# Kernel optimization log

Hardware: AMD Instinct MI355X
Metric: run time of the kernel (lower is better)

Reference implementation:

```python
import jax, jax.numpy as jnp
import numpy as np

EMBED_DIM = 1024
NUM_HEADS = 16
D_K = EMBED_DIM // NUM_HEADS
GAMMA = 1.0


def setup_inputs() -> dict:
    key = jax.random.key(0)
    ks = jax.random.split(key, 5)
    B, N, E = 2, 2048, EMBED_DIM
    scale = 1.0 / np.sqrt(E)
    x = jax.random.normal(ks[0], (B, N, E), dtype=jnp.float32)
    Wq = jax.random.normal(ks[1], (E, E), dtype=jnp.float32) * scale
    Wk = jax.random.normal(ks[2], (E, E), dtype=jnp.float32) * scale
    Wv = jax.random.normal(ks[3], (E, E), dtype=jnp.float32) * scale
    Wo = jax.random.normal(ks[4], (E, E), dtype=jnp.float32) * scale
    mask = jnp.ones((B, N), dtype=jnp.int32)
    return {"x": x, "Wq": Wq, "Wk": Wk, "Wv": Wv, "Wo": Wo, "mask": mask}


def _split_heads(t):
    B, N, E = t.shape
    return t.reshape(B, N, NUM_HEADS, D_K).transpose(0, 2, 1, 3)  # [B,H,N,dk]


def reference(x, Wq, Wk, Wv, Wo, mask):
    B, N, E = x.shape
    # Linear layers (bias=False): y = x @ W.T
    q = _split_heads(x @ Wq.T)
    k = _split_heads(x @ Wk.T)
    v = _split_heads(x @ Wv.T)
    # Squared L2 distance via ||q||^2 + ||k||^2 - 2 q.k (same math as (q-k)^2.sum,
    # without materializing the [B,H,N,N,dk] diff tensor).
    q_sq = jnp.sum(q * q, axis=-1)  # [B,H,N]
    k_sq = jnp.sum(k * k, axis=-1)  # [B,H,N]
    qk = jnp.einsum('bhqd,bhkd->bhqk', q, k)
    sq_dist = jnp.maximum(q_sq[..., :, None] + k_sq[..., None, :] - 2.0 * qk, 0.0)
    similarity = jnp.exp(-GAMMA * sq_dist)  # [B,H,N,N]
    # mask.unsqueeze(1).unsqueeze(2): broadcast over heads and query dim
    mask_exp = mask[:, None, None, :]  # [B,1,1,N]
    similarity = jnp.where(mask_exp == 0, jnp.float32(-1e9), similarity)
    attn = jax.nn.softmax(similarity, axis=-1)
    # dropout p=0.0 (eval) -> identity
    out = jnp.einsum('bhqk,bhkd->bhqd', attn, v)
    out = out.transpose(0, 2, 1, 3).reshape(B, N, E)
    return out @ Wo.T
```

## Files before the change

kernel.cpp:

```cpp
#include <hip/hip_runtime.h>
#include <hip/hip_bf16.h>


using bf16x8 = __attribute__((ext_vector_type(8))) __bf16;
using f32x4  = __attribute__((ext_vector_type(4))) float;
using f32x16 = __attribute__((ext_vector_type(16))) float;

typedef const __attribute__((address_space(1))) void* gas_t;
typedef __attribute__((address_space(3))) void* las_t;

#define C_LOG2E 1.4426950408889634f
#define TWO_C   2.8853900817779268f
#define NEG_INV_4C (-0.17328679513998632f)

#if __has_builtin(__builtin_amdgcn_exp2f)
#define EXP2(x) __builtin_amdgcn_exp2f(x)
#else
#define EXP2(x) __expf((x) * 0.6931471805599453f)
#endif

static __device__ __forceinline__ unsigned short f2bf(float x) {
  union { float f; unsigned u; } c; c.f = x;
  unsigned u = c.u;
  u += 0x7fffu + ((u >> 16) & 1u);
  return (unsigned short)(u >> 16);
}
static __device__ __forceinline__ float bf2f(unsigned short b) {
  union { unsigned u; float f; } c; c.u = ((unsigned)b) << 16;
  return c.f;
}
static __device__ __forceinline__ unsigned cvt_pk_bf16(float lo, float hi) {
  unsigned r;
  asm("v_cvt_pk_bf16_f32 %0, %1, %2" : "=v"(r) : "v"(lo), "v"(hi));
  return r;
}
static __device__ __forceinline__ void permlane32_swap(unsigned &a, unsigned &b) {
#if __has_builtin(__builtin_amdgcn_permlane32_swap)
  auto r = __builtin_amdgcn_permlane32_swap(a, b, false, false);
  a = r[0]; b = r[1];
#else
  asm("v_permlane32_swap_b32 %0, %1" : "+v"(a), "+v"(b));
#endif
}

#define SYNC_VM(N)                                                           \
  do {                                                                       \
    asm volatile("s_waitcnt vmcnt(" #N ") lgkmcnt(0)\n\ts_barrier" ::: "memory"); \
    __builtin_amdgcn_sched_barrier(0);                                       \
  } while (0)

__global__ __launch_bounds__(256)
void cvt_all(const float* __restrict__ x,  const float* __restrict__ wq,
             const float* __restrict__ wk, const float* __restrict__ wv,
             const float* __restrict__ wo,
             unsigned short* __restrict__ xbf, unsigned short* __restrict__ Wbf,
             float* __restrict__ FullVm, float* __restrict__ den_base,
             unsigned* __restrict__ kmax_bits) {
  const int idx = blockIdx.x * 256 + threadIdx.x;
  if (blockIdx.x == 0) {
    const int tid = threadIdx.x;
#pragma unroll
    for (int i = 0; i < 8; ++i) FullVm[tid + i * 256] = 0.f;
    if (tid < 32) kmax_bits[tid] = 0xFF800000u;
    if (tid < 2) den_base[tid] = 0.f;
  }
  const float* src; unsigned short* dst; int off;
  if (idx < 1048576) { src = x; dst = xbf; off = idx; }
  else {
    const int r = idx - 1048576;
    const int w = r >> 18;
    off = r & 262143;
    src = (w == 0) ? wq : (w == 1) ? wk : (w == 2) ? wv : wo;
    dst = Wbf + (size_t)w * 1048576u;
  }
  const float4 v = ((const float4*)src)[off];
  ushort4 o;
  o.x = f2bf(v.x); o.y = f2bf(v.y); o.z = f2bf(v.z); o.w = f2bf(v.w);
  ((ushort4*)dst)[off] = o;
}

template<int MODE>
__global__ __launch_bounds__(256)
void gemm_bt(const unsigned short* __restrict__ A,
             const unsigned short* __restrict__ Bt,
             void* __restrict__ out0, int Kdim,
             float* __restrict__ qsqp, float* __restrict__ ksqp) {
  constexpr int RING = (MODE == 0) ? 3 : 4;
  __shared__ unsigned short As[RING][4096];
  __shared__ unsigned short Bs[RING][4096];
  const int t  = threadIdx.x;
  const int m0 = blockIdx.x * 128;
  const int n0 = blockIdx.y * 128;
  const int srow = t >> 2;
  const int scol = (((t & 3) ^ (srow & 3) ^ ((srow >> 2) & 3))) * 8;
  const unsigned short* pA = A  + (size_t)(m0 + srow) * Kdim + scol;
  const unsigned short* pB = Bt + (size_t)(n0 + srow) * Kdim + scol;
  const size_t rowskip = (size_t)64 * Kdim;

  const int wave = t >> 6, lane = t & 63;
  const int wm = (wave >> 1) * 64, wn = (wave & 1) * 64;
  const int fr = lane & 15, fg = lane >> 4;
  const int fswz = fg ^ (fr & 3) ^ ((fr >> 2) & 3);
  const int aoff = (wm + fr) * 32 + fswz * 8;
  const int boff = (wn + fr) * 32 + fswz * 8;

  f32x4 acc[4][4];
#pragma unroll
  for (int mi = 0; mi < 4; ++mi)
#pragma unroll
    for (int ni = 0; ni < 4; ++ni)
      acc[mi][ni] = (f32x4){0.f, 0.f, 0.f, 0.f};

#define GSTAGE(bi, kk)                                                                                  \
  do {                                                                                                  \
    const int kc = (kk) * 32;                                                                           \
    __builtin_amdgcn_global_load_lds((gas_t)(const void*)(pA + kc),           (las_t)(void*)(As[bi] + t * 8),        16, 0, 0); \
    __builtin_amdgcn_global_load_lds((gas_t)(const void*)(pA + kc + rowskip), (las_t)(void*)(As[bi] + 2048 + t * 8), 16, 0, 0); \
    __builtin_amdgcn_global_load_lds((gas_t)(const void*)(pB + kc),           (las_t)(void*)(Bs[bi] + t * 8),        16, 0, 0); \
    __builtin_amdgcn_global_load_lds((gas_t)(const void*)(pB + kc + rowskip), (las_t)(void*)(Bs[bi] + 2048 + t * 8), 16, 0, 0); \
  } while (0)

  const int NK = Kdim >> 5;
  if constexpr (MODE == 0) {
    GSTAGE(0, 0);
    GSTAGE(1, 1);
    for (int ks = 0; ks < NK; ++ks) {
      const int cur = ks % 3;
      if (ks + 1 < NK) SYNC_VM(4); else SYNC_VM(0);
      if (ks + 2 < NK) GSTAGE((ks + 2) % 3, ks + 2);

      bf16x8 af[4], bfr[4];
#pragma unroll
      for (int mi = 0; mi < 4; ++mi) af[mi]  = *(const bf16x8*)(As[cur] + aoff + mi * 512);
#pragma unroll
      for (int ni = 0; ni < 4; ++ni) bfr[ni] = *(const bf16x8*)(Bs[cur] + boff + ni * 512);
#pragma unroll
      for (int mi = 0; mi < 4; ++mi)
#pragma unroll
        for (int ni = 0; ni < 4; ++ni)
          acc[mi][ni] = __builtin_amdgcn_mfma_f32_16x16x32_bf16(af[mi], bfr[ni], acc[mi][ni], 0, 0, 0);
    }
  } else {
    GSTAGE(0, 0);
    GSTAGE(1, 1);
    GSTAGE(2, 2);
    for (int ks = 0; ks < NK; ++ks) {
      const int cur = ks & 3;
      if (ks + 2 < NK) SYNC_VM(8);
      else if (ks + 1 < NK) SYNC_VM(4);
      else SYNC_VM(0);
      if (ks + 3 < NK) GSTAGE((ks + 3) & 3, ks + 3);

      bf16x8 af[4], bfr[4];
#pragma unroll
      for (int mi = 0; mi < 4; ++mi) af[mi]  = *(const bf16x8*)(As[cur] + aoff + mi * 512);
#pragma unroll
      for (int ni = 0; ni < 4; ++ni) bfr[ni] = *(const bf16x8*)(Bs[cur] + boff + ni * 512);
#pragma unroll
      for (int mi = 0; mi < 4; ++mi)
#pragma unroll
        for (int ni = 0; ni < 4; ++ni)
          acc[mi][ni] = __builtin_amdgcn_mfma_f32_16x16x32_bf16(af[mi], bfr[ni], acc[mi][ni], 0, 0, 0);
    }
  }
#undef GSTAGE

  if constexpr (MODE == 1) {
    float* dst = (float*)out0;
#pragma unroll
    for (int mi = 0; mi < 4; ++mi) {
      const int gm = m0 + wm + mi * 16 + fg * 4;
#pragma unroll
      for (int ni = 0; ni < 4; ++ni) {
        const int gn = n0 + wn + ni * 16 + fr;
#pragma unroll
        for (int r = 0; r < 4; ++r)
          dst[(size_t)(gm + r) * 1024 + gn] = acc[mi][ni][r];
      }
    }
    return;
  } else {
    const int wavecol = n0 + wn;
    const int zz = wavecol >> 10;
    unsigned short* outw = (unsigned short*)out0;
    if (zz < 2) {
      const float sc = (zz == 0) ? TWO_C : 1.0f;
      const float qscale = (zz == 0) ? NEG_INV_4C : -C_LOG2E;
      unsigned short* dst = outw + (size_t)zz * 4194304u;
      const int hh = (wavecol & 1023) >> 6;
      float* dq = (zz == 0) ? qsqp : ksqp;
#pragma unroll
      for (int mi = 0; mi < 4; ++mi) {
        const int gm = m0 + wm + mi * 16 + fg * 4;
        float s0 = 0.f, s1 = 0.f, s2 = 0.f, s3 = 0.f;
#pragma unroll
        for (int ni = 0; ni < 4; ++ni) {
          const int col = (wavecol + ni * 16 + fr) & 1023;
          const unsigned short u0 = f2bf(acc[mi][ni][0] * sc);
          const unsigned short u1 = f2bf(acc[mi][ni][1] * sc);
          const unsigned short u2 = f2bf(acc[mi][ni][2] * sc);
          const unsigned short u3 = f2bf(acc[mi][ni][3] * sc);
          dst[(size_t)(gm + 0) * 1024 + col] = u0;
          dst[(size_t)(gm + 1) * 1024 + col] = u1;
          dst[(size_t)(gm + 2) * 1024 + col] = u2;
          dst[(size_t)(gm + 3) * 1024 + col] = u3;
          const float r0 = bf2f(u0), r1 = bf2f(u1), r2 = bf2f(u2), r3 = bf2f(u3);
          s0 += r0 * r0; s1 += r1 * r1; s2 += r2 * r2; s3 += r3 * r3;
        }
#pragma unroll
        for (int off2 = 1; off2 < 16; off2 <<= 1) {
          s0 += __shfl_xor(s0, off2);
          s1 += __shfl_xor(s1, off2);
          s2 += __shfl_xor(s2, off2);
          s3 += __shfl_xor(s3, off2);
        }
        if (fr == 0) {
          const int bb = gm >> 11;
          float4 o4;
          o4.x = s0 * qscale; o4.y = s1 * qscale;
          o4.z = s2 * qscale; o4.w = s3 * qscale;
          *(float4*)(dq + (bb * 16 + hh) * 2048 + (gm & 2047)) = o4;
        }
      }
    } else {
#pragma unroll
      for (int mi = 0; mi < 4; ++mi) {
        const int gm = m0 + wm + mi * 16 + fg * 4;
#pragma unroll
        for (int ni = 0; ni < 4; ++ni) {
          const int gn = n0 + wn + ni * 16 + fr;
          const int col = gn & 1023;
          ushort4 o4;
          o4.x = f2bf(acc[mi][ni][0]); o4.y = f2bf(acc[mi][ni][1]);
          o4.z = f2bf(acc[mi][ni][2]); o4.w = f2bf(acc[mi][ni][3]);
          const int bb = gm >> 11, nn = gm & 2047;
          const int hh = col >> 6, dd = col & 63;
          unsigned short* vt = outw + (size_t)2 * 4194304u;
          *(ushort4*)(vt + ((size_t)((bb * 16 + hh) * 64 + dd)) * 2048 + nn) = o4;
        }
      }
    }
  }
}

__global__ __launch_bounds__(256)
void prep_kernel(const unsigned short* __restrict__ Vt,
                 const int* __restrict__ mask,
                 const float* __restrict__ ksqp,
                 float* __restrict__ maskf,
                 float* __restrict__ FullVm,
                 float* __restrict__ den_base,
                 unsigned* __restrict__ kmax_bits) {
  const int bh = blockIdx.x >> 3, c = blockIdx.x & 7;
  const int b = bh >> 4;
  const int wave = threadIdx.x >> 6, lane = threadIdx.x & 63;
  const int k0 = c * 256;
  const int4 mi4 = *(const int4*)(mask + b * 2048 + k0 + lane * 4);
  const float mvx = mi4.x ? 1.f : 0.f, mvy = mi4.y ? 1.f : 0.f;
  const float mvz = mi4.z ? 1.f : 0.f, mvw = mi4.w ? 1.f : 0.f;
#pragma unroll 4
  for (int dr = wave * 16; dr < wave * 16 + 16; ++dr) {
    const ushort4 v = *(const ushort4*)(Vt + ((size_t)bh * 64 + dr) * 2048 + k0 + lane * 4);
    float s = bf2f(v.x) * mvx + bf2f(v.y) * mvy + bf2f(v.z) * mvz + bf2f(v.w) * mvw;
#pragma unroll
    for (int off = 32; off >= 1; off >>= 1) s += __shfl_xor(s, off);
    if (lane == 0) atomicAdd(&FullVm[bh * 64 + dr], s);
  }
  if (wave == 0) {
    const float4 kq = *(const float4*)(ksqp + bh * 2048 + k0 + lane * 4);
    float mx = fmaxf(fmaxf(kq.x, kq.y), fmaxf(kq.z, kq.w));
#pragma unroll
    for (int off = 32; off >= 1; off >>= 1) mx = fmaxf(mx, __shfl_xor(mx, off));
    if (lane == 0) atomicMin(&kmax_bits[bh], __float_as_uint(mx));
  }
  if (wave == 1 && (bh & 15) == 0) {
    float4 mf; mf.x = mvx; mf.y = mvy; mf.z = mvz; mf.w = mvw;
    *(float4*)(maskf + b * 2048 + k0 + lane * 4) = mf;
  }
  if (wave == 2 && (bh & 15) == 0) {
    float s = mvx + mvy + mvz + mvw;
#pragma unroll
    for (int off = 32; off >= 1; off >>= 1) s += __shfl_xor(s, off);
    if (lane == 0) atomicAdd(&den_base[b], s);
  }
}

__global__ __launch_bounds__(128)
void attn_kernel(const unsigned short* __restrict__ Qbf,
                 const unsigned short* __restrict__ Kbf,
                 const unsigned short* __restrict__ Vt,
                 const float* __restrict__ qsqp,
                 const float* __restrict__ ksqp,
                 const float* __restrict__ maskf,
                 const float* __restrict__ FullVm,
                 const float* __restrict__ den_base,
                 const float* __restrict__ kmaxb,
                 unsigned short* __restrict__ Obf) {
  __shared__ unsigned short Ks[4][4096];

  const int bh = blockIdx.x;
  const int b = bh >> 4, h = bh & 15;
  const int t = threadIdx.x;
  const int wave = t >> 6, lane = t & 63;
  const int li = lane & 31, hi = lane >> 5;
  const int q0 = blockIdx.y * 64 + wave * 32;
  const int qrow = q0 + li;

  const unsigned short* Qr = Qbf + (size_t)(b * 2048 + qrow) * 1024 + h * 64 + hi * 8;
  bf16x8 qf[4];
#pragma unroll
  for (int dblk = 0; dblk < 4; ++dblk) qf[dblk] = *(const bf16x8*)(Qr + dblk * 16);

  const float qsl = qsqp[bh * 2048 + qrow];
  const float thr = -14.0f - qsl - kmaxb[bh];

  const unsigned short* Kbase = Kbf + (size_t)b * 2048 * 1024 + h * 64;
  const unsigned short* VtB = Vt + (size_t)bh * 64 * 2048;

  const int p0 = t,        r0 = p0 >> 3, c0 = (p0 & 7) ^ (r0 & 7);
  const int p1 = 128 + t,  r1 = p1 >> 3, c1 = (p1 & 7) ^ (r1 & 7);
  const int p2 = 256 + t,  r2 = p2 >> 3, c2 = (p2 & 7) ^ (r2 & 7);
  const int p3 = 384 + t,  r3 = p3 >> 3, c3 = (p3 & 7) ^ (r3 & 7);

  f32x16 oa0, oa1;
#pragma unroll
  for (int r = 0; r < 16; ++r) { oa0[r] = 0.f; oa1[r] = 0.f; }
  float den = 0.f;

#define STAGE(bi, tj)                                                                               \
  do {                                                                                              \
    const int j0s = (tj) * 64;                                                                      \
    __builtin_amdgcn_global_load_lds((gas_t)(const void*)(Kbase + (size_t)(j0s + r0) * 1024 + c0 * 8), \
                                     (las_t)(void*)(Ks[bi] + p0 * 8), 16, 0, 0);                    \
    __builtin_amdgcn_global_load_lds((gas_t)(const void*)(Kbase + (size_t)(j0s + r1) * 1024 + c1 * 8), \
                                     (las_t)(void*)(Ks[bi] + p1 * 8), 16, 0, 0);                    \
    __builtin_amdgcn_global_load_lds((gas_t)(const void*)(Kbase + (size_t)(j0s + r2) * 1024 + c2 * 8), \
                                     (las_t)(void*)(Ks[bi] + p2 * 8), 16, 0, 0);                    \
    __builtin_amdgcn_global_load_lds((gas_t)(const void*)(Kbase + (size_t)(j0s + r3) * 1024 + c3 * 8), \
                                     (las_t)(void*)(Ks[bi] + p3 * 8), 16, 0, 0);                    \
  } while (0)

  STAGE(0, 0);
  STAGE(1, 1);
  STAGE(2, 2);

  const int ksw = li & 7;

  for (int tj = 0; tj < 32; ++tj) {
    const int cur = tj & 3;
    if (tj + 2 < 32) SYNC_VM(8);
    else if (tj + 1 < 32) SYNC_VM(4);
    else SYNC_VM(0);
    if (tj + 3 < 32) STAGE((tj + 3) & 3, tj + 3);

#pragma unroll
    for (int s = 0; s < 2; ++s) {
      const unsigned short* Krow = Ks[cur] + (s * 32 + li) * 64;
      f32x16 st;
#pragma unroll
      for (int r = 0; r < 16; ++r) st[r] = 0.f;
#pragma unroll
      for (int dblk = 0; dblk < 4; ++dblk) {
        const bf16x8 kf = *(const bf16x8*)(Krow + ((dblk * 2 + hi) ^ ksw) * 8);
        st = __builtin_amdgcn_mfma_f32_32x32x16_bf16(kf, qf[dblk], st, 0, 0, 0);
      }

      const float a0 = fmaxf(fmaxf(st[0], st[1]), st[2]);
      const float a1 = fmaxf(fmaxf(st[3], st[4]), st[5]);
      const float a2 = fmaxf(fmaxf(st[6], st[7]), st[8]);
      const float a3 = fmaxf(fmaxf(st[9], st[10]), st[11]);
      const float a4 = fmaxf(fmaxf(st[12], st[13]), st[14]);
      const float a5 = fmaxf(fmaxf(a0, a1), st[15]);
      const float a6 = fmaxf(fmaxf(a2, a3), a4);
      const float lmax = fmaxf(a5, a6);

      if (__any(lmax > thr)) {
        const int j0 = tj * 64 + s * 32;
        const float* ksb2 = ksqp + bh * 2048 + j0 + 4 * hi;
        const float* mfb2 = maskf + b * 2048 + j0 + 4 * hi;
        const float4 kq0 = *(const float4*)(ksb2);
        const float4 kq1 = *(const float4*)(ksb2 + 8);
        const float4 kq2 = *(const float4*)(ksb2 + 16);
        const float4 kq3 = *(const float4*)(ksb2 + 24);
        const float4 mf0 = *(const float4*)(mfb2);
        const float4 mf1 = *(const float4*)(mfb2 + 8);
        const float4 mf2 = *(const float4*)(mfb2 + 16);
        const float4 mf3 = *(const float4*)(mfb2 + 24);
        const float kqa[16] = {kq0.x, kq0.y, kq0.z, kq0.w, kq1.x, kq1.y, kq1.z, kq1.w,
                               kq2.x, kq2.y, kq2.z, kq2.w, kq3.x, kq3.y, kq3.z, kq3.w};
        const float mfa[16] = {mf0.x, mf0.y, mf0.z, mf0.w, mf1.x, mf1.y, mf1.z, mf1.w,
                               mf2.x, mf2.y, mf2.z, mf2.w, mf3.x, mf3.y, mf3.z, mf3.w};
        float dsv[16];
#pragma unroll
        for (int r = 0; r < 16; ++r) {
          const float z = __builtin_fminf(st[r] + qsl + kqa[r], 0.f);
          const float sx = EXP2(z);
          float pl = __builtin_fmaf(sx, 1.f / 120.f, 1.f / 24.f);
          pl = __builtin_fmaf(sx, pl, 1.f / 6.f);
          pl = __builtin_fmaf(sx, pl, 0.5f);
          pl = __builtin_fmaf(sx, pl, 1.f);
          const float d_ = sx * pl * mfa[r];
          dsv[r] = d_;
          den += d_;
        }

        unsigned u00 = cvt_pk_bf16(dsv[0],  dsv[1]);
        unsigned u01 = cvt_pk_bf16(dsv[2],  dsv[3]);
        unsigned u10 = cvt_pk_bf16(dsv[4],  dsv[5]);
        unsigned u11 = cvt_pk_bf16(dsv[6],  dsv[7]);
        unsigned u20 = cvt_pk_bf16(dsv[8],  dsv[9]);
        unsigned u21 = cvt_pk_bf16(dsv[10], dsv[11]);
        unsigned u30 = cvt_pk_bf16(dsv[12], dsv[13]);
        unsigned u31 = cvt_pk_bf16(dsv[14], dsv[15]);
        permlane32_swap(u00, u10);
        permlane32_swap(u01, u11);
        permlane32_swap(u20, u30);
        permlane32_swap(u21, u31);
        union { unsigned u[4]; bf16x8 v; } pf0, pf1;
        pf0.u[0] = u00; pf0.u[1] = u01; pf0.u[2] = u10; pf0.u[3] = u11;
        pf1.u[0] = u20; pf1.u[1] = u21; pf1.u[2] = u30; pf1.u[3] = u31;

#pragma unroll
        for (int dh = 0; dh < 2; ++dh) {
          const unsigned short* Vrow = VtB + (size_t)(dh * 32 + li) * 2048 + j0;
          const bf16x8 vf0 = *(const bf16x8*)(Vrow + hi * 8);
          const bf16x8 vf1 = *(const bf16x8*)(Vrow + 16 + hi * 8);
          if (dh == 0) {
            oa0 = __builtin_amdgcn_mfma_f32_32x32x16_bf16(vf0, pf0.v, oa0, 0, 0, 0);
            oa0 = __builtin_amdgcn_mfma_f32_32x32x16_bf16(vf1, pf1.v, oa0, 0, 0, 0);
          } else {
            oa1 = __builtin_amdgcn_mfma_f32_32x32x16_bf16(vf0, pf0.v, oa1, 0, 0, 0);
            oa1 = __builtin_amdgcn_mfma_f32_32x32x16_bf16(vf1, pf1.v, oa1, 0, 0, 0);
          }
        }
      }
    }
  }
#undef STAGE

  den += __shfl_xor(den, 32);
  const float inv = 1.f / (den_base[b] + den);
  const float* fvm = FullVm + bh * 64;
  unsigned short* orow = Obf + (size_t)(b * 2048 + qrow) * 1024 + h * 64;
#pragma unroll
  for (int dh = 0; dh < 2; ++dh)
#pragma unroll
    for (int w = 0; w < 4; ++w) {
      float v0, v1, v2, v3;
      if (dh == 0) {
        v0 = oa0[4 * w];     v1 = oa0[4 * w + 1];
        v2 = oa0[4 * w + 2]; v3 = oa0[4 * w + 3];
      } else {
        v0 = oa1[4 * w];     v1 = oa1[4 * w + 1];
        v2 = oa1[4 * w + 2]; v3 = oa1[4 * w + 3];
      }
      const float4 fv = *(const float4*)(fvm + dh * 32 + w * 8 + hi * 4);
      ushort4 o4;
      o4.x = f2bf((v0 + fv.x) * inv);
      o4.y = f2bf((v1 + fv.y) * inv);
      o4.z = f2bf((v2 + fv.z) * inv);
      o4.w = f2bf((v3 + fv.w) * inv);
      *(ushort4*)(orow + dh * 32 + w * 8 + hi * 4) = o4;
    }
}

extern "C" void kernel_launch(void* const* d_in, const int* in_sizes, int n_in,
                              void* d_out, int out_size, void* d_ws, size_t ws_size,
                              hipStream_t stream) {
  const float* x  = (const float*)d_in[0];
  const float* Wq = (const float*)d_in[1];
  const float* Wk = (const float*)d_in[2];
  const float* Wv = (const float*)d_in[3];
  const float* Wo = (const float*)d_in[4];
  const int* mask = (const int*)d_in[5];

  unsigned short* ws = (unsigned short*)d_ws;
  const size_t SZ = 4194304;
  unsigned short* xbf = ws;
  unsigned short* Wbf = ws + SZ;
  unsigned short* Qbf = ws + 2 * SZ;
  unsigned short* Kbf = ws + 3 * SZ;
  unsigned short* Vt  = ws + 4 * SZ;
  unsigned short* Obf = ws + 5 * SZ;
  float* qsqp = (float*)(ws + 6 * SZ);
  float* ksqp = qsqp + 65536;
  float* maskf = ksqp + 65536;
  float* FullVm = maskf + 4096;
  float* den_base = FullVm + 2048;
  float* kmaxb = den_base + 2;

  cvt_all<<<8192, 256, 0, stream>>>(x, Wq, Wk, Wv, Wo, xbf, Wbf,
                                    FullVm, den_base, (unsigned*)kmaxb);

  gemm_bt<0><<<dim3(32, 24), 256, 0, stream>>>(xbf, Wbf, Qbf, 1024, qsqp, ksqp);

  prep_kernel<<<256, 256, 0, stream>>>(Vt, mask, ksqp, maskf, FullVm, den_base,
                                       (unsigned*)kmaxb);

  attn_kernel<<<dim3(32, 32), 128, 0, stream>>>(Qbf, Kbf, Vt, qsqp, ksqp, maskf,
                                                FullVm, den_base, kmaxb, Obf);

  gemm_bt<1><<<dim3(32, 8), 256, 0, stream>>>(Obf, Wbf + 3145728, d_out, 1024,
                                              nullptr, nullptr);
}
```

Measured before the change: 108.5 us.

## Fold prep kernel reductions into conversion and QKV GEMM epilogues

Removes the separate prep kernel. Mask conversion and mask-count sums move into block 0 of the conversion kernel. The per-head k-norm minimum is computed with atomics in the K epilogue of the projection GEMM, and the masked column sums of V are accumulated in its V epilogue. This saves one launch and a re-read of V from global memory. In exchange it adds atomics and extra arithmetic to the GEMM epilogue, and block 0 of the conversion kernel does serial extra work.

```diff
diff --git a/kernel.cpp b/kernel.cpp
--- a/kernel.cpp
+++ b/kernel.cpp
@@ -52,8 +52,9 @@
 __global__ __launch_bounds__(256)
 void cvt_all(const float* __restrict__ x,  const float* __restrict__ wq,
              const float* __restrict__ wk, const float* __restrict__ wv,
-             const float* __restrict__ wo,
+             const float* __restrict__ wo, const int* __restrict__ mask,
              unsigned short* __restrict__ xbf, unsigned short* __restrict__ Wbf,
+             float* __restrict__ maskf,
              float* __restrict__ FullVm, float* __restrict__ den_base,
              unsigned* __restrict__ kmax_bits) {
   const int idx = blockIdx.x * 256 + threadIdx.x;
@@ -63,6 +64,22 @@
     for (int i = 0; i < 8; ++i) FullVm[tid + i * 256] = 0.f;
     if (tid < 32) kmax_bits[tid] = 0xFF800000u;
     if (tid < 2) den_base[tid] = 0.f;
+    __syncthreads();
+    float s0 = 0.f, s1 = 0.f;
+    for (int i = tid; i < 4096; i += 256) {
+      const float mv = (mask[i] == 0) ? 0.f : 1.f;
+      maskf[i] = mv;
+      if (i < 2048) s0 += mv; else s1 += mv;
+    }
+#pragma unroll
+    for (int off = 32; off >= 1; off >>= 1) {
+      s0 += __shfl_xor(s0, off);
+      s1 += __shfl_xor(s1, off);
+    }
+    if ((tid & 63) == 0) {
+      atomicAdd(&den_base[0], s0);
+      atomicAdd(&den_base[1], s1);
+    }
   }
   const float* src; unsigned short* dst; int off;
   if (idx < 1048576) { src = x; dst = xbf; off = idx; }
@@ -84,7 +101,10 @@
 void gemm_bt(const unsigned short* __restrict__ A,
              const unsigned short* __restrict__ Bt,
              void* __restrict__ out0, int Kdim,
-             float* __restrict__ qsqp, float* __restrict__ ksqp) {
+             float* __restrict__ qsqp, float* __restrict__ ksqp,
+             const float* __restrict__ maskf,
+             float* __restrict__ FullVm,
+             unsigned* __restrict__ kmax_bits) {
   constexpr int RING = (MODE == 0) ? 3 : 4;
   __shared__ unsigned short As[RING][4096];
   __shared__ unsigned short Bs[RING][4096];
@@ -220,12 +240,21 @@
           o4.x = s0 * qscale; o4.y = s1 * qscale;
           o4.z = s2 * qscale; o4.w = s3 * qscale;
           *(float4*)(dq + (bb * 16 + hh) * 2048 + (gm & 2047)) = o4;
+          if (zz == 1) {
+            const float mx = fmaxf(fmaxf(o4.x, o4.y), fmaxf(o4.z, o4.w));
+            atomicMin(kmax_bits + (bb * 16 + hh), __float_as_uint(mx));
+          }
         }
       }
     } else {
+      const int bb = (m0 + wm) >> 11;
+      const int hh = (wavecol & 1023) >> 6;
+      float fvp[4] = {0.f, 0.f, 0.f, 0.f};
 #pragma unroll
       for (int mi = 0; mi < 4; ++mi) {
         const int gm = m0 + wm + mi * 16 + fg * 4;
+        const int nn = gm & 2047;
+        const float4 mv = *(const float4*)(maskf + bb * 2048 + nn);
 #pragma unroll
         for (int ni = 0; ni < 4; ++ni) {
           const int gn = n0 + wn + ni * 16 + fr;
@@ -233,55 +262,24 @@
           ushort4 o4;
           o4.x = f2bf(acc[mi][ni][0]); o4.y = f2bf(acc[mi][ni][1]);
           o4.z = f2bf(acc[mi][ni][2]); o4.w = f2bf(acc[mi][ni][3]);
-          const int bb = gm >> 11, nn = gm & 2047;
-          const int hh = col >> 6, dd = col & 63;
+          const int dd = col & 63;
           unsigned short* vt = outw + (size_t)2 * 4194304u;
           *(ushort4*)(vt + ((size_t)((bb * 16 + hh) * 64 + dd)) * 2048 + nn) = o4;
+          fvp[ni] += mv.x * bf2f(o4.x) + mv.y * bf2f(o4.y) +
+                     mv.z * bf2f(o4.z) + mv.w * bf2f(o4.w);
         }
       }
-    }
-  }
-}
-
-__global__ __launch_bounds__(256)
-void prep_kernel(const unsigned short* __restrict__ Vt,
-                 const int* __restrict__ mask,
-                 const float* __restrict__ ksqp,
-                 float* __restrict__ maskf,
-                 float* __restrict__ FullVm,
-                 float* __restrict__ den_base,
-                 unsigned* __restrict__ kmax_bits) {
-  const int bh = blockIdx.x >> 3, c = blockIdx.x & 7;
-  const int b = bh >> 4;
-  const int wave = threadIdx.x >> 6, lane = threadIdx.x & 63;
-  const int k0 = c * 256;
-  const int4 mi4 = *(const int4*)(mask + b * 2048 + k0 + lane * 4);
-  const float mvx = mi4.x ? 1.f : 0.f, mvy = mi4.y ? 1.f : 0.f;
-  const float mvz = mi4.z ? 1.f : 0.f, mvw = mi4.w ? 1.f : 0.f;
-#pragma unroll 4
-  for (int dr = wave * 16; dr < wave * 16 + 16; ++dr) {
-    const ushort4 v = *(const ushort4*)(Vt + ((size_t)bh * 64 + dr) * 2048 + k0 + lane * 4);
-    float s = bf2f(v.x) * mvx + bf2f(v.y) * mvy + bf2f(v.z) * mvz + bf2f(v.w) * mvw;
-#pragma unroll
-    for (int off = 32; off >= 1; off >>= 1) s += __shfl_xor(s, off);
-    if (lane == 0) atomicAdd(&FullVm[bh * 64 + dr], s);
-  }
-  if (wave == 0) {
-    const float4 kq = *(const float4*)(ksqp + bh * 2048 + k0 + lane * 4);
-    float mx = fmaxf(fmaxf(kq.x, kq.y), fmaxf(kq.z, kq.w));
-#pragma unroll
-    for (int off = 32; off >= 1; off >>= 1) mx = fmaxf(mx, __shfl_xor(mx, off));
-    if (lane == 0) atomicMin(&kmax_bits[bh], __float_as_uint(mx));
-  }
-  if (wave == 1 && (bh & 15) == 0) {
-    float4 mf; mf.x = mvx; mf.y = mvy; mf.z = mvz; mf.w = mvw;
-    *(float4*)(maskf + b * 2048 + k0 + lane * 4) = mf;
-  }
-  if (wave == 2 && (bh & 15) == 0) {
-    float s = mvx + mvy + mvz + mvw;
-#pragma unroll
-    for (int off = 32; off >= 1; off >>= 1) s += __shfl_xor(s, off);
-    if (lane == 0) atomicAdd(&den_base[b], s);
+#pragma unroll
+      for (int ni = 0; ni < 4; ++ni) {
+        fvp[ni] += __shfl_xor(fvp[ni], 16);
+        fvp[ni] += __shfl_xor(fvp[ni], 32);
+      }
+      if (fg == 0) {
+#pragma unroll
+        for (int ni = 0; ni < 4; ++ni)
+          atomicAdd(&FullVm[(bb * 16 + hh) * 64 + ni * 16 + fr], fvp[ni]);
+      }
+    }
   }
 }
 
@@ -489,17 +487,16 @@
   float* den_base = FullVm + 2048;
   float* kmaxb = den_base + 2;
 
-  cvt_all<<<8192, 256, 0, stream>>>(x, Wq, Wk, Wv, Wo, xbf, Wbf,
-                                    FullVm, den_base, (unsigned*)kmaxb);
-
-  gemm_bt<0><<<dim3(32, 24), 256, 0, stream>>>(xbf, Wbf, Qbf, 1024, qsqp, ksqp);
-
-  prep_kernel<<<256, 256, 0, stream>>>(Vt, mask, ksqp, maskf, FullVm, den_base,
-                                       (unsigned*)kmaxb);
+  cvt_all<<<8192, 256, 0, stream>>>(x, Wq, Wk, Wv, Wo, mask, xbf, Wbf,
+                                    maskf, FullVm, den_base, (unsigned*)kmaxb);
+
+  gemm_bt<0><<<dim3(32, 24), 256, 0, stream>>>(xbf, Wbf, Qbf, 1024, qsqp, ksqp,
+                                               maskf, FullVm, (unsigned*)kmaxb);
 
   attn_kernel<<<dim3(32, 32), 128, 0, stream>>>(Qbf, Kbf, Vt, qsqp, ksqp, maskf,
                                                 FullVm, den_base, kmaxb, Obf);
 
   gemm_bt<1><<<dim3(32, 8), 256, 0, stream>>>(Obf, Wbf + 3145728, d_out, 1024,
-                                              nullptr, nullptr);
-}
+                                              nullptr, nullptr, nullptr, nullptr,
+                                              nullptr);
+}
```

Measured after the change: 204.9 us. 1.89x slower.
